# Kernel tuning notes

Measured on AMD Instinct MI355X. Metric: run time of the kernel, lower is better.

Reference implementation:

```python
import jax, jax.numpy as jnp
import numpy as np

N = 50000      # nodes
E = 800000     # edges (avg degree 16)
G = 8          # graphs in batch
D = 128        # in/hidden feats
C = 10         # classes


def setup_inputs() -> dict:
    key = jax.random.key(0)
    ks = jax.random.split(key, 9)
    x = jax.random.normal(ks[0], (N, D), dtype=jnp.float32)
    edge_index = jax.random.randint(ks[1], (2, E), 0, N)
    node2graph = jnp.sort(jax.random.randint(ks[2], (N,), 0, G))
    s = 1.0 / np.sqrt(D)
    W1 = jax.random.normal(ks[3], (D, D), dtype=jnp.float32) * s
    b1 = jnp.zeros((D,), jnp.float32)
    W2 = jax.random.normal(ks[4], (D, D), dtype=jnp.float32) * s
    b2 = jnp.zeros((D,), jnp.float32)
    Wl = jax.random.normal(ks[5], (D, C), dtype=jnp.float32) * s
    bl = jnp.zeros((C,), jnp.float32)
    return {"x": x, "edge_index": edge_index, "node2graph": node2graph,
            "W1": W1, "b1": b1, "W2": W2, "b2": b2, "Wl": Wl, "bl": bl}


def _graph_conv(h, src, dst, out_isqrt, in_isqrt, W, b):
    # DGL GraphConv, norm='both': D_in^{-1/2} A D_out^{-1/2} (h W) + b
    h = (h * out_isqrt[:, None]) @ W
    agg = jax.ops.segment_sum(h[src], dst, num_segments=N)  # SpMM gather/scatter
    return agg * in_isqrt[:, None] + b


def reference(x, edge_index, node2graph, W1, b1, W2, b2, Wl, bl):
    src, dst = edge_index[0], edge_index[1]
    ones_e = jnp.ones((E,), jnp.float32)
    out_deg = jnp.clip(jax.ops.segment_sum(ones_e, src, num_segments=N), 1.0)
    in_deg = jnp.clip(jax.ops.segment_sum(ones_e, dst, num_segments=N), 1.0)
    out_isqrt = jax.lax.rsqrt(out_deg)
    in_isqrt = jax.lax.rsqrt(in_deg)

    h = jax.nn.relu(_graph_conv(x, src, dst, out_isqrt, in_isqrt, W1, b1))
    h = jax.nn.relu(_graph_conv(h, src, dst, out_isqrt, in_isqrt, W2, b2))

    # AvgPooling: per-graph mean of node features
    sums = jax.ops.segment_sum(h, node2graph, num_segments=G)
    counts = jnp.clip(jax.ops.segment_sum(jnp.ones((N,), jnp.float32), node2graph, num_segments=G), 1.0)
    hg = sums / counts[:, None]

    logits = hg @ Wl + bl
    return jax.nn.softmax(logits, axis=1)
```

## Files before the change

kernel.cpp:

```cpp
#include <hip/hip_runtime.h>
#include <stdint.h>

#define FD 128
#define NG 8
#define NC 10
#define MAXB 1024
#define CHUNK 4096
#define BFPAD 4

typedef __attribute__((ext_vector_type(8))) short bf16x8;
typedef __attribute__((ext_vector_type(4))) float f32x4;
typedef __attribute__((ext_vector_type(2))) float f32x2;

__device__ __forceinline__ float bf2f(uint16_t u){
    union { uint32_t i; float f; } v; v.i = ((uint32_t)u) << 16; return v.f;
}
__device__ __forceinline__ uint16_t f2bf(float f){
    union { float f; uint32_t i; } v; v.f = f;
    uint32_t r = v.i + 0x7fff + ((v.i >> 16) & 1);
    return (uint16_t)(r >> 16);
}

#if __has_builtin(__builtin_amdgcn_cvt_pk_f32_fp8) && __has_builtin(__builtin_amdgcn_cvt_pk_fp8_f32)
__device__ __forceinline__ f32x2 fp8lo2f(uint32_t p){
    return __builtin_amdgcn_cvt_pk_f32_fp8((int)p, false);
}
__device__ __forceinline__ f32x2 fp8hi2f(uint32_t p){
    return __builtin_amdgcn_cvt_pk_f32_fp8((int)p, true);
}
__device__ __forceinline__ uint32_t pk4fp8(float a, float b, float c, float d){
    int u = 0;
    u = __builtin_amdgcn_cvt_pk_fp8_f32(a, b, u, false);
    u = __builtin_amdgcn_cvt_pk_fp8_f32(c, d, u, true);
    return (uint32_t)u;
}
#else
__device__ __forceinline__ float fp8tof(uint32_t b){
    union { uint32_t i; float f; } v;
    v.i = ((b & 0x7f) << 20) | ((b & 0x80) << 24);
    return v.f * 0x1p120f;
}
__device__ __forceinline__ f32x2 fp8lo2f(uint32_t p){
    return (f32x2){fp8tof(p & 0xff), fp8tof((p >> 8) & 0xff)};
}
__device__ __forceinline__ f32x2 fp8hi2f(uint32_t p){
    return (f32x2){fp8tof((p >> 16) & 0xff), fp8tof((p >> 24) & 0xff)};
}
__device__ __forceinline__ uint32_t f2fp8(float f){
    union { float f; uint32_t i; } v; v.f = f;
    uint32_t s = (v.i >> 24) & 0x80;
    float a = fabsf(f);
    if (a < 0x1p-10f) return s;
    if (a > 448.f) return s | 0x7e;
    v.f = a;
    uint32_t r = v.i + 0x7ffff + ((v.i >> 20) & 1);
    int e = (int)(r >> 23) - 127 + 7;
    uint32_t m = (r >> 20) & 7;
    if (e <= 0){
        uint32_t q = (uint32_t)(a * 512.f + 0.5f);
        return s | (q > 7 ? 8 : q);
    }
    if (e > 15) return s | 0x7e;
    return s | ((uint32_t)e << 3) | m;
}
__device__ __forceinline__ uint32_t pk4fp8(float a, float b, float c, float d){
    return (uint32_t)f2fp8(a) | ((uint32_t)f2fp8(b)<<8) |
           ((uint32_t)f2fp8(c)<<16) | ((uint32_t)f2fp8(d)<<24);
}
#endif

__global__ __launch_bounds__(256) void k_prep(const float* __restrict__ W1,
        const float* __restrict__ W2, uint16_t* Wf1, uint16_t* Wf2,
        int B, int* __restrict__ bfD, int* __restrict__ bfS,
        float* __restrict__ pool){
    int t = threadIdx.x;
    int id = blockIdx.x*256 + t;
    {
        int w = id >> 14;
        int r = id & 16383;
        int j = r & 7, frag = r >> 3;
        int lane = frag & 63, t2 = frag >> 6;
        int n = t2 & 7, kk = t2 >> 3;
        int k = kk*32 + (lane>>4)*8 + j;
        int col = n*16 + (lane&15);
        float v = (w ? W2 : W1)[k*128 + col];
        (w ? Wf2 : Wf1)[r] = f2bf(v);
    }
    for (int i = id; i < B*BFPAD; i += 32768){ bfD[i] = 0; bfS[i] = 0; }
    if (id < NG*FD) pool[id] = 0.f;
}

__global__ __launch_bounds__(1024) void k_gemm_scatter(const int* __restrict__ ei,
        int E, int B, int shift, int CAP, int C,
        int* __restrict__ bfD, int* __restrict__ bfS,
        uint32_t* __restrict__ tempD, uint16_t* __restrict__ tempS,
        const float* __restrict__ X, const uint16_t* __restrict__ Wf,
        uint8_t* __restrict__ out8, int N){
    __shared__ __align__(16) char lds[45056];
    int t = threadIdx.x;
    int lmask = (1<<shift) - 1;
    if ((int)blockIdx.x < C){
        uint32_t* payD = (uint32_t*)lds;
        uint16_t* payS = (uint16_t*)lds;
        int* cnt  = (int*)(lds + 28672);
        int* off  = cnt  + MAXB;
        int* resv = off  + MAXB;
        int* scr  = resv + MAXB;
        int c = blockIdx.x;
        int e0 = c*CHUNK, e1 = min(E, e0+CHUNK);
        int ss[4], dd[4];
        #pragma unroll
        for (int k=0;k<4;k++){
            int e = e0 + t + k*1024;
            bool ok = e < e1;
            ss[k] = ok ? ei[e]   : -1;
            dd[k] = ok ? ei[E+e] : -1;
        }
        for (int i=t;i<7168;i+=1024) payD[i] = 0xFFFFFFFFu;
        for (int i=t;i<B;i+=1024) cnt[i] = 0;
        __syncthreads();
        int bb[4], pl[4];
        #pragma unroll
        for (int k=0;k<4;k++){
            bb[k] = -1;
            if (dd[k] >= 0){
                int b = dd[k] >> shift;
                bb[k] = b;
                pl[k] = atomicAdd(&cnt[b], 1);
            }
        }
        __syncthreads();
        int v = (t < B) ? ((cnt[t]+3) & ~3) : 0;
        scr[t] = v; __syncthreads();
        for (int o=1;o<1024;o<<=1){ int u=(t>=o)?scr[t-o]:0; __syncthreads(); scr[t]+=u; __syncthreads(); }
        if (t < B) off[t] = scr[t] - v;
        __syncthreads();
        int totalPad = scr[1023];
        #pragma unroll
        for (int k=0;k<4;k++)
            if (bb[k] >= 0)
                payD[off[bb[k]] + pl[k]] = ((uint32_t)(dd[k] & lmask) << 20) | (uint32_t)ss[k];
        for (int b=t;b<B;b+=1024){
            int pc = (cnt[b]+3) & ~3;
            resv[b] = pc ? atomicAdd(&bfD[b*BFPAD], pc) : 0;
        }
        __syncthreads();
        for (int g=t; g < (totalPad>>2); g += 1024){
            int pos = g << 2;
            int lo = 0, hi = B-1;
            while (lo < hi){ int mid=(lo+hi+1)>>1; if (off[mid] <= pos) lo = mid; else hi = mid-1; }
            int rel = resv[lo] + (pos - off[lo]);
            if (rel + 4 <= CAP){
                uint4 w4 = *(const uint4*)&payD[pos];
                *(uint4*)&tempD[(size_t)lo*CAP + rel] = w4;
            }
        }
        __syncthreads();
        for (int i=t;i<11264;i+=1024) payS[i] = 0xFFFF;
        for (int i=t;i<B;i+=1024) cnt[i] = 0;
        __syncthreads();
        #pragma unroll
        for (int k=0;k<4;k++){
            bb[k] = -1;
            if (ss[k] >= 0){
                int b = ss[k] >> shift;
                bb[k] = b;
                pl[k] = atomicAdd(&cnt[b], 1);
            }
        }
        __syncthreads();
        v = (t < B) ? ((cnt[t]+7) & ~7) : 0;
        scr[t] = v; __syncthreads();
        for (int o=1;o<1024;o<<=1){ int u=(t>=o)?scr[t-o]:0; __syncthreads(); scr[t]+=u; __syncthreads(); }
        if (t < B) off[t] = scr[t] - v;
        __syncthreads();
        totalPad = scr[1023];
        #pragma unroll
        for (int k=0;k<4;k++)
            if (bb[k] >= 0) payS[off[bb[k]] + pl[k]] = (uint16_t)(ss[k] & lmask);
        for (int b=t;b<B;b+=1024){
            int pc = (cnt[b]+7) & ~7;
            resv[b] = pc ? atomicAdd(&bfS[b*BFPAD], pc) : 0;
        }
        __syncthreads();
        for (int g=t; g < (totalPad>>3); g += 1024){
            int pos = g << 3;
            int lo = 0, hi = B-1;
            while (lo < hi){ int mid=(lo+hi+1)>>1; if (off[mid] <= pos) lo = mid; else hi = mid-1; }
            int rel = resv[lo] + (pos - off[lo]);
            if (rel + 8 <= CAP){
                uint4 w4 = *(const uint4*)&payS[pos];
                *(uint4*)&tempS[(size_t)lo*CAP + rel] = w4;
            }
        }
        return;
    }
    int wave = t>>6, lane = t&63, quad = lane>>4, low = lane&15;
    int rowA  = (blockIdx.x - C)*256 + wave*16 + low;
    int rowAc = min(rowA, N-1);
    const float* arow = X + (size_t)rowAc*FD;
    bf16x8 ah[4];
    #pragma unroll
    for (int kk=0;kk<4;kk++){
        f32x4 f0 = *(const f32x4*)(arow + kk*32 + quad*8);
        f32x4 f1 = *(const f32x4*)(arow + kk*32 + quad*8 + 4);
        #pragma unroll
        for (int j=0;j<4;j++) ah[kk][j]   = (short)f2bf(f0[j]);
        #pragma unroll
        for (int j=0;j<4;j++) ah[kk][j+4] = (short)f2bf(f1[j]);
    }
    f32x4 acc[8];
    #pragma unroll
    for (int n=0;n<8;n++) acc[n] = (f32x4){0.f,0.f,0.f,0.f};
    #pragma unroll
    for (int kk=0;kk<4;kk++){
        #pragma unroll
        for (int n=0;n<8;n++){
            bf16x8 bh = *(const bf16x8*)(Wf + ((size_t)((kk*8+n)*64 + lane))*8);
            acc[n] = __builtin_amdgcn_mfma_f32_16x16x32_bf16(bh, ah[kk], acc[n], 0, 0, 0);
        }
    }
    if (rowA < N){
        uint8_t* orow = out8 + (size_t)rowA*FD;
        #pragma unroll
        for (int n=0;n<8;n++){
            uint32_t pk = pk4fp8(acc[n][0], acc[n][1], acc[n][2], acc[n][3]);
            *(uint32_t*)(orow + n*16 + quad*4) = pk;
        }
    }
}

__global__ __launch_bounds__(256) void k_build(const uint32_t* __restrict__ tempD,
        const uint16_t* __restrict__ tempS,
        const int* __restrict__ bfD, const int* __restrict__ bfS,
        int B, int shift, int N, int CAP,
        int* __restrict__ row_off, int* __restrict__ deg_in,
        float* __restrict__ isqo, int* __restrict__ csr){
    __shared__ int cnt_[MAXB];
    __shared__ int off_[MAXB];
    int b = blockIdx.x, t = threadIdx.x;
    int range = 1<<shift, nb0 = b<<shift;
    int fill = min(bfD[b*BFPAD], CAP);
    const uint32_t* seg = tempD + (size_t)b*CAP;
    for (int i=t;i<range;i+=256) cnt_[i]=0;
    __syncthreads();
    for (int i=t;i<fill;i+=256){
        int loc = (int)(seg[i] >> 20);
        if (loc < range) atomicAdd(&cnt_[loc], 1);
    }
    __syncthreads();
    if (range == 64){
        if (t < 64){
            int v = cnt_[t];
            int inc = v;
            #pragma unroll
            for (int o=1;o<64;o<<=1){
                int u = __shfl_up(inc, o);
                if (t >= o) inc += u;
            }
            off_[t] = inc - v;
        }
    } else if (t == 0){
        int run = 0;
        for (int i=0;i<range;i++){ off_[i]=run; run+=cnt_[i]; }
    }
    __syncthreads();
    int base = b*CAP;
    for (int i=t;i<range;i+=256){
        int node = nb0 + i;
        if (node < N){
            row_off[node] = base + off_[i];
            deg_in[node]  = cnt_[i];
        }
    }
    __syncthreads();
    int* csrb = csr + (size_t)base;
    for (int i=t;i<fill;i+=256){
        uint32_t v = seg[i];
        int loc = (int)(v >> 20);
        if (loc < range){
            int p = atomicAdd(&off_[loc], 1);
            csrb[p] = (int)(v & 0xFFFFFu);
        }
    }
    __syncthreads();
    for (int i=t;i<range;i+=256) cnt_[i]=0;
    __syncthreads();
    int fillS = min(bfS[b*BFPAD], CAP);
    const uint16_t* segS = tempS + (size_t)b*CAP;
    for (int i=t;i<fillS;i+=256){
        int v = (int)segS[i];
        if (v < range) atomicAdd(&cnt_[v], 1);
    }
    __syncthreads();
    for (int i=t;i<range;i+=256){
        int node = nb0 + i;
        if (node < N) isqo[node] = rsqrtf((float)max(cnt_[i], 1));
    }
}

template<bool WSCALE>
__device__ __forceinline__ void spmm_row(const uint2* __restrict__ tp,
        const int* __restrict__ csr_src, const float* __restrict__ isqo,
        int e0, int e1, int l, int qb,
        f32x2& a01, f32x2& a23, f32x2& a45, f32x2& a67){
    for (int base = e0; base < e1; base += 16){
        int my = 0;
        if (base + l < e1) my = csr_src[base + l];
        int cnt = min(16, e1 - base);
        for (int j0 = 0; j0 < cnt; j0 += 8){
            int ss[8];
            #pragma unroll
            for (int k=0;k<8;k++)
                ss[k] = __shfl(my, qb + min(j0 + k, cnt-1));
            uint2 p[8]; float w[8];
            #pragma unroll
            for (int k=0;k<8;k++)
                p[k] = tp[(size_t)ss[k]*16 + l];
            if (WSCALE){
                #pragma unroll
                for (int k=0;k<8;k++) w[k] = isqo[ss[k]];
            }
            #pragma unroll
            for (int k=0;k<8;k++){
                if (j0 + k < cnt){
                    if (WSCALE){
                        a01 += fp8lo2f(p[k].x)*w[k]; a23 += fp8hi2f(p[k].x)*w[k];
                        a45 += fp8lo2f(p[k].y)*w[k]; a67 += fp8hi2f(p[k].y)*w[k];
                    } else {
                        a01 += fp8lo2f(p[k].x); a23 += fp8hi2f(p[k].x);
                        a45 += fp8lo2f(p[k].y); a67 += fp8hi2f(p[k].y);
                    }
                }
            }
        }
    }
}

__global__ __launch_bounds__(256, 6) void k_spmm_gemm(const uint8_t* __restrict__ tmp8,
        const int* __restrict__ row_off, const int* __restrict__ deg_in,
        const int* __restrict__ csr_src, const float* __restrict__ isqo,
        const float* __restrict__ bias, const uint16_t* __restrict__ Wf,
        uint8_t* __restrict__ out8, int N){
    __shared__ __align__(16) uint16_t hsrow[32][136];
    int tid = threadIdx.x;
    int l = tid & 15, qid = tid >> 4, qb = (tid & 63) & 48;
    const uint2* tp = (const uint2*)tmp8;
    f32x4 bv0 = *(const f32x4*)(bias + l*8);
    f32x4 bv1 = *(const f32x4*)(bias + l*8 + 4);
    #pragma unroll
    for (int i = 0; i < 2; i++){
        int rowL = qid*2 + i;
        int node = blockIdx.x*32 + rowL;
        int e0 = 0, e1 = 0;
        if (node < N){ e0 = row_off[node]; e1 = e0 + deg_in[node]; }
        f32x2 a01={0.f,0.f}, a23={0.f,0.f}, a45={0.f,0.f}, a67={0.f,0.f};
        spmm_row<true>(tp, csr_src, isqo, e0, e1, l, qb, a01, a23, a45, a67);
        float isq = rsqrtf((float)max(e1 - e0, 1));
        float r0 = fmaxf(a01.x*isq + bv0[0], 0.f);
        float r1 = fmaxf(a01.y*isq + bv0[1], 0.f);
        float r2 = fmaxf(a23.x*isq + bv0[2], 0.f);
        float r3 = fmaxf(a23.y*isq + bv0[3], 0.f);
        float r4 = fmaxf(a45.x*isq + bv1[0], 0.f);
        float r5 = fmaxf(a45.y*isq + bv1[1], 0.f);
        float r6 = fmaxf(a67.x*isq + bv1[2], 0.f);
        float r7 = fmaxf(a67.y*isq + bv1[3], 0.f);
        uint4 o;
        o.x = (uint32_t)f2bf(r0) | ((uint32_t)f2bf(r1) << 16);
        o.y = (uint32_t)f2bf(r2) | ((uint32_t)f2bf(r3) << 16);
        o.z = (uint32_t)f2bf(r4) | ((uint32_t)f2bf(r5) << 16);
        o.w = (uint32_t)f2bf(r6) | ((uint32_t)f2bf(r7) << 16);
        if (node >= N) o = (uint4){0u,0u,0u,0u};
        *(uint4*)(&hsrow[rowL][l*8]) = o;
    }
    __syncthreads();
    int wave = tid>>6, lane = tid&63, quad = lane>>4, low = lane&15;
    int rowL = (wave&1)*16 + low;
    int rowA = blockIdx.x*32 + rowL;
    int nb0 = (wave>>1)*4;
    bf16x8 ah[4];
    #pragma unroll
    for (int kk=0;kk<4;kk++)
        ah[kk] = *(const bf16x8*)(&hsrow[rowL][kk*32 + quad*8]);
    f32x4 acc[4];
    #pragma unroll
    for (int n=0;n<4;n++) acc[n] = (f32x4){0.f,0.f,0.f,0.f};
    #pragma unroll
    for (int kk=0;kk<4;kk++){
        #pragma unroll
        for (int n2=0;n2<4;n2++){
            int n = nb0 + n2;
            bf16x8 bh = *(const bf16x8*)(Wf + ((size_t)((kk*8+n)*64 + lane))*8);
            acc[n2] = __builtin_amdgcn_mfma_f32_16x16x32_bf16(bh, ah[kk], acc[n2], 0, 0, 0);
        }
    }
    if (rowA < N){
        float sc = isqo[rowA];
        uint8_t* orow = out8 + (size_t)rowA*FD;
        #pragma unroll
        for (int n2=0;n2<4;n2++){
            int n = nb0 + n2;
            uint32_t pk = pk4fp8(acc[n2][0]*sc, acc[n2][1]*sc, acc[n2][2]*sc, acc[n2][3]*sc);
            *(uint32_t*)(orow + n*16 + quad*4) = pk;
        }
    }
}

__global__ __launch_bounds__(256, 6) void k_spmm_pool(const uint8_t* __restrict__ tmp8,
        const int* __restrict__ row_off, const int* __restrict__ deg_in,
        const int* __restrict__ csr_src,
        const float* __restrict__ bias, const int* __restrict__ n2g,
        float* __restrict__ pool, int N){
    __shared__ float sacc[NG*FD];
    int tid = threadIdx.x;
    for (int i = tid; i < NG*FD; i += 256) sacc[i] = 0.f;
    __syncthreads();
    int l = tid & 15, qid = tid >> 4, qb = (tid & 63) & 48;
    const uint2* tp = (const uint2*)tmp8;
    f32x4 bv0 = *(const f32x4*)(bias + l*8);
    f32x4 bv1 = *(const f32x4*)(bias + l*8 + 4);
    int rg = -1;
    float racc[8];
    #pragma unroll
    for (int j=0;j<8;j++) racc[j] = 0.f;
    #pragma unroll
    for (int i = 0; i < 2; i++){
        int node = blockIdx.x*32 + qid*2 + i;
        if (node < N){
            int e0 = row_off[node], e1 = e0 + deg_in[node];
            f32x2 a01={0.f,0.f}, a23={0.f,0.f}, a45={0.f,0.f}, a67={0.f,0.f};
            spmm_row<false>(tp, csr_src, nullptr, e0, e1, l, qb, a01, a23, a45, a67);
            float isq = rsqrtf((float)max(e1 - e0, 1));
            float r[8];
            r[0] = fmaxf(a01.x*isq + bv0[0], 0.f);
            r[1] = fmaxf(a01.y*isq + bv0[1], 0.f);
            r[2] = fmaxf(a23.x*isq + bv0[2], 0.f);
            r[3] = fmaxf(a23.y*isq + bv0[3], 0.f);
            r[4] = fmaxf(a45.x*isq + bv1[0], 0.f);
            r[5] = fmaxf(a45.y*isq + bv1[1], 0.f);
            r[6] = fmaxf(a67.x*isq + bv1[2], 0.f);
            r[7] = fmaxf(a67.y*isq + bv1[3], 0.f);
            int g = n2g[node];
            if (g != rg){
                if (rg >= 0){
                    #pragma unroll
                    for (int j=0;j<8;j++) atomicAdd(&sacc[rg*FD + l*8 + j], racc[j]);
                }
                rg = g;
                #pragma unroll
                for (int j=0;j<8;j++) racc[j] = 0.f;
            }
            #pragma unroll
            for (int j=0;j<8;j++) racc[j] += r[j];
        }
    }
    if (rg >= 0){
        #pragma unroll
        for (int j=0;j<8;j++) atomicAdd(&sacc[rg*FD + l*8 + j], racc[j]);
    }
    __syncthreads();
    for (int i = tid; i < NG*FD; i += 256){
        float v = sacc[i];
        if (v != 0.f) atomicAdd(&pool[i], v);
    }
}

__global__ __launch_bounds__(128) void k_final(const float* __restrict__ pool,
        const int* __restrict__ n2g, int N, const float* __restrict__ Wl,
        const float* __restrict__ bl, float* __restrict__ out){
    __shared__ int ub[NG+1];
    __shared__ float logits[NG][NC];
    int t = threadIdx.x;
    if (t <= NG){
        int lo = 0, hi = N;
        while (lo < hi){ int mid = (lo+hi)>>1; if (n2g[mid] < t) lo = mid+1; else hi = mid; }
        ub[t] = lo;
    }
    __syncthreads();
    if (t < NG*NC){
        int g = t/NC, c = t%NC;
        float cnt = (float)max(ub[g+1]-ub[g], 1);
        float inv = 1.f/cnt;
        float acc = bl[c];
        for (int d=0; d<FD; d++)
            acc += pool[g*FD+d]*inv * Wl[d*NC+c];
        logits[g][c] = acc;
    }
    __syncthreads();
    if (t < NG*NC){
        int g = t/NC, c = t%NC;
        float m = -1e30f;
        for (int i=0;i<NC;i++) m = fmaxf(m, logits[g][i]);
        float ssum = 0.f;
        for (int i=0;i<NC;i++) ssum += expf(logits[g][i]-m);
        out[t] = expf(logits[g][c]-m)/ssum;
    }
}

extern "C" void kernel_launch(void* const* d_in, const int* in_sizes, int n_in,
                              void* d_out, int out_size, void* d_ws, size_t ws_size,
                              hipStream_t stream) {
    const float* x   = (const float*)d_in[0];
    const int*   ei  = (const int*)d_in[1];
    const int*   n2g = (const int*)d_in[2];
    const float* W1  = (const float*)d_in[3];
    const float* b1  = (const float*)d_in[4];
    const float* W2  = (const float*)d_in[5];
    const float* b2  = (const float*)d_in[6];
    const float* Wl  = (const float*)d_in[7];
    const float* bl  = (const float*)d_in[8];
    float* outp = (float*)d_out;

    int N = in_sizes[2];
    int E = in_sizes[1] / 2;

    int shift = 6;
    while ((((N + (1<<shift) - 1) >> shift) > MAXB) && shift < 10) shift++;
    int B = (N + (1<<shift) - 1) >> shift;
    int C = (E + CHUNK - 1) / CHUNK;
    int meanFill = (int)(((long long)E << shift) / (N > 0 ? N : 1)) + 1;
    int CAP = 4096;
    while (CAP < 3*meanFill) CAP <<= 1;

    char* w = (char*)d_ws;
    size_t off = 0;
    auto alloc = [&](size_t bytes)->char*{ char* p = w + off; off += (bytes + 255) & ~(size_t)255; return p; };
    float*    pool    = (float*)alloc((size_t)NG*FD*4);
    int*      deg_in  = (int*)alloc((size_t)N*4);
    int*      row_off = (int*)alloc((size_t)N*4);
    float*    isqo    = (float*)alloc((size_t)N*4);
    int*      bfD     = (int*)alloc((size_t)MAXB*BFPAD*4);
    int*      bfS     = (int*)alloc((size_t)MAXB*BFPAD*4);
    uint16_t* Wf1     = (uint16_t*)alloc(16384*2);
    uint16_t* Wf2     = (uint16_t*)alloc(16384*2);
    uint32_t* tempD   = (uint32_t*)alloc((size_t)B*CAP*4);
    uint16_t* tempS   = (uint16_t*)alloc((size_t)B*CAP*2);
    int*      csr     = (int*)alloc((size_t)B*CAP*4);
    uint8_t*  tmp8    = (uint8_t*)alloc((size_t)N*FD);
    uint8_t*  tmp8b   = (uint8_t*)alloc((size_t)N*FD);
    (void)ws_size;

    int gb2 = (N + 255)/256;
    int gb  = (N + 31)/32;

    k_prep        <<<128,       256,  0, stream>>>(W1, W2, Wf1, Wf2, B, bfD, bfS, pool);
    k_gemm_scatter<<<C + gb2,   1024, 0, stream>>>(ei, E, B, shift, CAP, C,
                                                   bfD, bfS, tempD, tempS,
                                                   x, Wf1, tmp8, N);
    k_build       <<<B,         256,  0, stream>>>(tempD, tempS, bfD, bfS, B, shift, N, CAP,
                                                   row_off, deg_in, isqo, csr);
    k_spmm_gemm   <<<gb,        256,  0, stream>>>(tmp8,  row_off, deg_in, csr, isqo, b1, Wf2, tmp8b, N);
    k_spmm_pool   <<<gb,        256,  0, stream>>>(tmp8b, row_off, deg_in, csr, b2, n2g, pool, N);
    k_final       <<<1,         128,  0, stream>>>(pool, n2g, N, Wl, bl, outp);
}
```

Baseline: 187.6 us.

## Fuse final softmax into pooling kernel via last-block counter; double scatter chunk

Removes the separate k_final launch: the pooling kernel now increments a global counter after its pool atomics, and the last block to finish computes the per-graph mean, the logits and the softmax. Separately, the edge-scatter chunk size goes from 4096 to 8192 edges per block, with LDS grown to hold twice the payload per block. This halves the number of scatter blocks and their global bucket atomics, at the cost of more LDS per block and less parallelism in that phase.

New measurement: 307.1 us. 63.7% more time.

```diff
diff --git a/kernel.cpp b/kernel.cpp
--- a/kernel.cpp
+++ b/kernel.cpp
@@ -5,7 +5,7 @@
 #define NG 8
 #define NC 10
 #define MAXB 1024
-#define CHUNK 4096
+#define CHUNK 8192
 #define BFPAD 4
 
 typedef __attribute__((ext_vector_type(8))) short bf16x8;
@@ -72,7 +72,7 @@
 __global__ __launch_bounds__(256) void k_prep(const float* __restrict__ W1,
         const float* __restrict__ W2, uint16_t* Wf1, uint16_t* Wf2,
         int B, int* __restrict__ bfD, int* __restrict__ bfS,
-        float* __restrict__ pool){
+        float* __restrict__ pool, int* __restrict__ ctr){
     int t = threadIdx.x;
     int id = blockIdx.x*256 + t;
     {
@@ -88,6 +88,7 @@
     }
     for (int i = id; i < B*BFPAD; i += 32768){ bfD[i] = 0; bfS[i] = 0; }
     if (id < NG*FD) pool[id] = 0.f;
+    if (id == 0) *ctr = 0;
 }
 
 __global__ __launch_bounds__(1024) void k_gemm_scatter(const int* __restrict__ ei,
@@ -96,32 +97,32 @@
         uint32_t* __restrict__ tempD, uint16_t* __restrict__ tempS,
         const float* __restrict__ X, const uint16_t* __restrict__ Wf,
         uint8_t* __restrict__ out8, int N){
-    __shared__ __align__(16) char lds[45056];
+    __shared__ __align__(16) char lds[61440];
     int t = threadIdx.x;
     int lmask = (1<<shift) - 1;
     if ((int)blockIdx.x < C){
         uint32_t* payD = (uint32_t*)lds;
         uint16_t* payS = (uint16_t*)lds;
-        int* cnt  = (int*)(lds + 28672);
+        int* cnt  = (int*)(lds + 45056);
         int* off  = cnt  + MAXB;
         int* resv = off  + MAXB;
         int* scr  = resv + MAXB;
         int c = blockIdx.x;
         int e0 = c*CHUNK, e1 = min(E, e0+CHUNK);
-        int ss[4], dd[4];
-        #pragma unroll
-        for (int k=0;k<4;k++){
+        int ss[8], dd[8];
+        #pragma unroll
+        for (int k=0;k<8;k++){
             int e = e0 + t + k*1024;
             bool ok = e < e1;
             ss[k] = ok ? ei[e]   : -1;
             dd[k] = ok ? ei[E+e] : -1;
         }
-        for (int i=t;i<7168;i+=1024) payD[i] = 0xFFFFFFFFu;
+        for (int i=t;i<11264;i+=1024) payD[i] = 0xFFFFFFFFu;
         for (int i=t;i<B;i+=1024) cnt[i] = 0;
         __syncthreads();
-        int bb[4], pl[4];
-        #pragma unroll
-        for (int k=0;k<4;k++){
+        int bb[8], pl[8];
+        #pragma unroll
+        for (int k=0;k<8;k++){
             bb[k] = -1;
             if (dd[k] >= 0){
                 int b = dd[k] >> shift;
@@ -137,7 +138,7 @@
         __syncthreads();
         int totalPad = scr[1023];
         #pragma unroll
-        for (int k=0;k<4;k++)
+        for (int k=0;k<8;k++)
             if (bb[k] >= 0)
                 payD[off[bb[k]] + pl[k]] = ((uint32_t)(dd[k] & lmask) << 20) | (uint32_t)ss[k];
         for (int b=t;b<B;b+=1024){
@@ -156,11 +157,11 @@
             }
         }
         __syncthreads();
-        for (int i=t;i<11264;i+=1024) payS[i] = 0xFFFF;
+        for (int i=t;i<15360;i+=1024) payS[i] = 0xFFFF;
         for (int i=t;i<B;i+=1024) cnt[i] = 0;
         __syncthreads();
         #pragma unroll
-        for (int k=0;k<4;k++){
+        for (int k=0;k<8;k++){
             bb[k] = -1;
             if (ss[k] >= 0){
                 int b = ss[k] >> shift;
@@ -176,7 +177,7 @@
         __syncthreads();
         totalPad = scr[1023];
         #pragma unroll
-        for (int k=0;k<4;k++)
+        for (int k=0;k<8;k++)
             if (bb[k] >= 0) payS[off[bb[k]] + pl[k]] = (uint16_t)(ss[k] & lmask);
         for (int b=t;b<B;b+=1024){
             int pc = (cnt[b]+7) & ~7;
@@ -410,8 +411,13 @@
         const int* __restrict__ row_off, const int* __restrict__ deg_in,
         const int* __restrict__ csr_src,
         const float* __restrict__ bias, const int* __restrict__ n2g,
-        float* __restrict__ pool, int N){
+        float* __restrict__ pool, int N,
+        const float* __restrict__ Wl, const float* __restrict__ bl,
+        float* __restrict__ out, int* __restrict__ ctr){
     __shared__ float sacc[NG*FD];
+    __shared__ int isLast;
+    __shared__ int ub[NG+1];
+    __shared__ float logits[NG][NC];
     int tid = threadIdx.x;
     for (int i = tid; i < NG*FD; i += 256) sacc[i] = 0.f;
     __syncthreads();
@@ -463,37 +469,38 @@
         float v = sacc[i];
         if (v != 0.f) atomicAdd(&pool[i], v);
     }
-}
-
-__global__ __launch_bounds__(128) void k_final(const float* __restrict__ pool,
-        const int* __restrict__ n2g, int N, const float* __restrict__ Wl,
-        const float* __restrict__ bl, float* __restrict__ out){
-    __shared__ int ub[NG+1];
-    __shared__ float logits[NG][NC];
-    int t = threadIdx.x;
-    if (t <= NG){
+    __threadfence();
+    if (tid == 0){
+        int done = __hip_atomic_fetch_add(ctr, 1, __ATOMIC_ACQ_REL, __HIP_MEMORY_SCOPE_AGENT);
+        isLast = (done == (int)gridDim.x - 1) ? 1 : 0;
+    }
+    __syncthreads();
+    if (!isLast) return;
+    if (tid <= NG){
         int lo = 0, hi = N;
-        while (lo < hi){ int mid = (lo+hi)>>1; if (n2g[mid] < t) lo = mid+1; else hi = mid; }
-        ub[t] = lo;
-    }
-    __syncthreads();
-    if (t < NG*NC){
-        int g = t/NC, c = t%NC;
-        float cnt = (float)max(ub[g+1]-ub[g], 1);
-        float inv = 1.f/cnt;
+        while (lo < hi){ int mid = (lo+hi)>>1; if (n2g[mid] < tid) lo = mid+1; else hi = mid; }
+        ub[tid] = lo;
+    }
+    __syncthreads();
+    if (tid < NG*NC){
+        int g = tid/NC, c = tid%NC;
+        float cntg = (float)max(ub[g+1]-ub[g], 1);
+        float inv = 1.f/cntg;
         float acc = bl[c];
-        for (int d=0; d<FD; d++)
-            acc += pool[g*FD+d]*inv * Wl[d*NC+c];
+        for (int d=0; d<FD; d++){
+            float pv = __hip_atomic_load(&pool[g*FD+d], __ATOMIC_RELAXED, __HIP_MEMORY_SCOPE_AGENT);
+            acc += pv*inv * Wl[d*NC+c];
+        }
         logits[g][c] = acc;
     }
     __syncthreads();
-    if (t < NG*NC){
-        int g = t/NC, c = t%NC;
+    if (tid < NG*NC){
+        int g = tid/NC, c = tid%NC;
         float m = -1e30f;
         for (int i=0;i<NC;i++) m = fmaxf(m, logits[g][i]);
         float ssum = 0.f;
         for (int i=0;i<NC;i++) ssum += expf(logits[g][i]-m);
-        out[t] = expf(logits[g][c]-m)/ssum;
+        out[tid] = expf(logits[g][c]-m)/ssum;
     }
 }
 
@@ -526,6 +533,7 @@
     size_t off = 0;
     auto alloc = [&](size_t bytes)->char*{ char* p = w + off; off += (bytes + 255) & ~(size_t)255; return p; };
     float*    pool    = (float*)alloc((size_t)NG*FD*4);
+    int*      ctr     = (int*)alloc(256);
     int*      deg_in  = (int*)alloc((size_t)N*4);
     int*      row_off = (int*)alloc((size_t)N*4);
     float*    isqo    = (float*)alloc((size_t)N*4);
@@ -543,13 +551,13 @@
     int gb2 = (N + 255)/256;
     int gb  = (N + 31)/32;
 
-    k_prep        <<<128,       256,  0, stream>>>(W1, W2, Wf1, Wf2, B, bfD, bfS, pool);
+    k_prep        <<<128,       256,  0, stream>>>(W1, W2, Wf1, Wf2, B, bfD, bfS, pool, ctr);
     k_gemm_scatter<<<C + gb2,   1024, 0, stream>>>(ei, E, B, shift, CAP, C,
                                                    bfD, bfS, tempD, tempS,
                                                    x, Wf1, tmp8, N);
     k_build       <<<B,         256,  0, stream>>>(tempD, tempS, bfD, bfS, B, shift, N, CAP,
                                                    row_off, deg_in, isqo, csr);
     k_spmm_gemm   <<<gb,        256,  0, stream>>>(tmp8,  row_off, deg_in, csr, isqo, b1, Wf2, tmp8b, N);
-    k_spmm_pool   <<<gb,        256,  0, stream>>>(tmp8b, row_off, deg_in, csr, b2, n2g, pool, N);
-    k_final       <<<1,         128,  0, stream>>>(pool, n2g, N, Wl, bl, outp);
-}
+    k_spmm_pool   <<<gb,        256,  0, stream>>>(tmp8b, row_off, deg_in, csr, b2, n2g, pool, N,
+                                                   Wl, bl, outp, ctr);
+}
```
